# Optimization experiments

Measured on AMD Instinct MI355X. Metric: run time of the kernel, lower is better.

Reference implementation:

```python
import jax, jax.numpy as jnp
import numpy as np

BM = 192  # query block size (kernel hard-coded to BM=192)


def setup_inputs() -> dict:
    key = jax.random.key(0)
    k1, k2, k3 = jax.random.split(key, 3)
    B, H, S, D = 1, 12, 3840, 128
    q = jax.random.normal(k1, (B, H, S, D), dtype=jnp.float32)
    k = jax.random.normal(k2, (B, H, S, D), dtype=jnp.float32)
    v = jax.random.normal(k3, (B, H, S, D), dtype=jnp.float32)
    topk = 1024
    return {"q": q, "k": k, "v": v, "topk": topk}


def reference(q, k, v, topk):
    # Chipmunk SparseDiffAttn core pipeline:
    # 1) dense_colsum_attn: dense attention whose probs are column-summed per
    #    192-query block to produce block scores bs [B,H,QG,S]
    # 2) topk index selection per query group (mask -> indices)
    # 3) csp_attn: block-sparse attention where each 192-query group attends
    #    only to its selected top-k keys
    B, H, S, D = q.shape
    QG = S // BM
    scale = 1.0 / np.sqrt(D)

    # --- dense colsum attention (scoring pass) ---
    scores = jnp.einsum('bhqd,bhkd->bhqk', q, k) * scale      # [B,H,S,S]
    probs = jax.nn.softmax(scores, axis=-1)                   # [B,H,S,S]
    # column-sum of attention probs within each 192-query block
    bs = probs.reshape(B, H, QG, BM, S).sum(axis=-2)          # [B,H,QG,S]

    # --- topk mask -> per-group key indices ---
    _, inds = jax.lax.top_k(bs, topk)                         # [B,H,QG,TK] int32

    # --- block-sparse gather attention (csp_attn) ---
    # gather selected keys/values per query group
    gather = jax.vmap(jax.vmap(lambda kv, idx: kv[idx]))      # over B, H
    kg = gather(k, inds)                                      # [B,H,QG,TK,D]
    vg = gather(v, inds)                                      # [B,H,QG,TK,D]
    qg = q.reshape(B, H, QG, BM, D)                           # [B,H,QG,BM,D]

    s2 = jnp.einsum('bhgqd,bhgkd->bhgqk', qg, kg) * scale     # [B,H,QG,BM,TK]
    p2 = jax.nn.softmax(s2, axis=-1)
    o = jnp.einsum('bhgqk,bhgkd->bhgqd', p2, vg)              # [B,H,QG,BM,D]
    return o.reshape(B, H, S, D)
```

## Files before the change

### kernel.cpp

```cpp
#include <hip/hip_runtime.h>
#include <math.h>


#define HH 12
#define SS 3840
#define DD 128
#define QGn 20
#define TKn 1024
#define NROWS (HH * QGn)
#define HS (HH * SS)
#define NT 60
#define TCH 3072
#define SCALE_D 0.08838834764831845
#define SCALE_F 0.08838834764831845f

typedef short short8 __attribute__((ext_vector_type(8)));
typedef short short4v __attribute__((ext_vector_type(4)));
typedef float f32x4 __attribute__((ext_vector_type(4)));

#define MFMA(a, b, c) __builtin_amdgcn_mfma_f32_16x16x32_bf16(a, b, c, 0, 0, 0)
#define MFMA_B16(c, a, b) \
  c = __builtin_amdgcn_mfma_f32_16x16x32_bf16(a, b, c, 0, 0, 0)

typedef __attribute__((address_space(3))) unsigned int lds_u32;
typedef const __attribute__((address_space(1))) unsigned int glb_u32;

__device__ __forceinline__ unsigned short bf_rne(float x) {
  unsigned u = __float_as_uint(x);
  u = (u + 0x7fffu + ((u >> 16) & 1u)) >> 16;
  return (unsigned short)u;
}
__device__ __forceinline__ float bf_f(unsigned short b) {
  return __uint_as_float(((unsigned)b) << 16);
}
__device__ __forceinline__ void split3(float f, unsigned short& a,
                                       unsigned short& b, unsigned short& c) {
  a = bf_rne(f);
  float r = f - bf_f(a);
  b = bf_rne(r);
  r = r - bf_f(b);
  c = bf_rne(r);
}
__device__ __forceinline__ void split2(float f, unsigned short& a,
                                       unsigned short& b) {
  a = bf_rne(f);
  float r = f - bf_f(a);
  b = bf_rne(r);
}
__device__ __forceinline__ short8 ldfrag(const unsigned short* base, int chunk) {
  return *(const short8*)&base[(size_t)chunk * 8];
}

__global__ __launch_bounds__(1024) void presplit_kernel(
    const float* __restrict__ q, const float* __restrict__ k,
    unsigned short* __restrict__ qsplit, unsigned short* __restrict__ ksplit) {
  const int t = threadIdx.x;
  const int lane = t & 63;
  const int u = t >> 6;
  const int kc = u & 3, kt = u >> 2;
  const int ln = lane & 15, quad = lane >> 4;
  const int c = blockIdx.x;
  const int h = blockIdx.y;
  const float* src = blockIdx.z ? k : q;
  unsigned short* dst = blockIdx.z ? ksplit : qsplit;

  const float* p =
      &src[(size_t)(h * SS + c * 64 + kt * 16 + ln) * DD + kc * 32 + quad * 8];
  float b8[8];
  *(float4*)&b8[0] = *(const float4*)&p[0];
  *(float4*)&b8[4] = *(const float4*)&p[4];
  unsigned short f0[8], f1[8], f2[8];
#pragma unroll
  for (int e = 0; e < 8; ++e) split3(b8[e], f0[e], f1[e], f2[e]);
  size_t base =
      ((size_t)(h * NT + c) * TCH + ((kt * 4 + kc) * 3) * 64 + lane) * 8;
  *(ushort4*)&dst[base + 0] = *(ushort4*)&f0[0];
  *(ushort4*)&dst[base + 4] = *(ushort4*)&f0[4];
  *(ushort4*)&dst[base + 512] = *(ushort4*)&f1[0];
  *(ushort4*)&dst[base + 516] = *(ushort4*)&f1[4];
  *(ushort4*)&dst[base + 1024] = *(ushort4*)&f2[0];
  *(ushort4*)&dst[base + 1028] = *(ushort4*)&f2[4];
}

__global__ __launch_bounds__(256) void stats_mfma(
    const unsigned short* __restrict__ qsplit,
    const unsigned short* __restrict__ ksplit,
    double* __restrict__ lpart) {
  __shared__ __align__(16) unsigned short Bs[3][6144];
  const int t = threadIdx.x;
  const int w = t >> 6;
  const int lane = t & 63;
  const int ln = lane & 15;
  const int quad = lane >> 4;
  const int h = blockIdx.y;
  const int nq = blockIdx.z;
  const int q0 = blockIdx.x * 128 + w * 32;
  const int tq = blockIdx.x * 2 + (w >> 1);
  const int ktA = (w & 1) * 2;

  short8 A[2][4][3];
  {
    const unsigned short* qb = &qsplit[(size_t)(h * NT + tq) * TCH * 8];
#pragma unroll
    for (int s = 0; s < 2; ++s)
#pragma unroll
      for (int kc = 0; kc < 4; ++kc)
#pragma unroll
        for (int cm = 0; cm < 3; ++cm)
          A[s][kc][cm] =
              ldfrag(qb, (((ktA + s) * 4 + kc) * 3 + cm) * 64 + lane);
  }

  double racc[2][4];
#pragma unroll
  for (int s = 0; s < 2; ++s)
#pragma unroll
    for (int r = 0; r < 4; ++r) racc[s][r] = 0.0;

  const unsigned short* kq = &ksplit[(size_t)(h * NT + nq * 15) * TCH * 8];

#define STG_S(slot, j)                                                     \
  do {                                                                     \
    const unsigned short* src_ = kq + (size_t)(j) * 6144 + t * 8;          \
    __builtin_amdgcn_global_load_lds((glb_u32*)(src_),                     \
        (lds_u32*)&Bs[slot][w * 512], 16, 0, 0);                           \
    __builtin_amdgcn_global_load_lds((glb_u32*)(src_ + 2048),              \
        (lds_u32*)&Bs[slot][2048 + w * 512], 16, 0, 0);                    \
    __builtin_amdgcn_global_load_lds((glb_u32*)(src_ + 4096),              \
        (lds_u32*)&Bs[slot][4096 + w * 512], 16, 0, 0);                    \
  } while (0)

  const f32x4 z = {0.f, 0.f, 0.f, 0.f};
  f32x4 C[2][3];

  STG_S(0, 0);

  int cur = 0;
#pragma unroll 1
  for (int j = 0; j < 60; ++j) {
    __builtin_amdgcn_sched_barrier(0);
    if (j < 59) {
      const int nxt = (cur == 2) ? 0 : cur + 1;
      STG_S(nxt, j + 1);
      asm volatile("s_waitcnt vmcnt(3)" ::: "memory");
    } else {
      asm volatile("s_waitcnt vmcnt(0)" ::: "memory");
    }
    __builtin_amdgcn_s_barrier();
    __builtin_amdgcn_sched_barrier(0);
    __builtin_amdgcn_s_setprio(1);
    if (j > 0) {
#pragma unroll
      for (int s = 0; s < 2; ++s)
#pragma unroll
        for (int r = 0; r < 4; ++r) {
          float sv = (C[s][0][r] + C[s][1][r]) + C[s][2][r];
          racc[s][r] += (double)__expf(sv * SCALE_F);
        }
    }
    const unsigned short* Bp = &Bs[cur][0];
#pragma unroll
    for (int kc = 0; kc < 4; ++kc) {
      short8 B0 = *(const short8*)&Bp[(kc * 3 + 0) * 512 + lane * 8];
      short8 B1 = *(const short8*)&Bp[(kc * 3 + 1) * 512 + lane * 8];
      short8 B2 = *(const short8*)&Bp[(kc * 3 + 2) * 512 + lane * 8];
#pragma unroll
      for (int s = 0; s < 2; ++s) {
        if (kc == 0) {
          C[s][0] = MFMA(A[s][0][0], B0, z);
          C[s][1] = MFMA(A[s][0][0], B1, z);
          C[s][1] = MFMA(A[s][0][1], B0, C[s][1]);
          C[s][0] = MFMA(A[s][0][1], B1, C[s][0]);
          C[s][2] = MFMA(A[s][0][2], B0, z);
          C[s][2] = MFMA(A[s][0][0], B2, C[s][2]);
        } else {
          MFMA_B16(C[s][0], A[s][kc][0], B0);
          MFMA_B16(C[s][1], A[s][kc][0], B1);
          MFMA_B16(C[s][1], A[s][kc][1], B0);
          MFMA_B16(C[s][0], A[s][kc][1], B1);
          MFMA_B16(C[s][2], A[s][kc][2], B0);
          MFMA_B16(C[s][2], A[s][kc][0], B2);
        }
      }
    }
    __builtin_amdgcn_s_setprio(0);
    cur = (cur == 2) ? 0 : cur + 1;
  }
#undef STG_S

#pragma unroll
  for (int s = 0; s < 2; ++s)
#pragma unroll
    for (int r = 0; r < 4; ++r) {
      float sv = (C[s][0][r] + C[s][1][r]) + C[s][2][r];
      racc[s][r] += (double)__expf(sv * SCALE_F);
    }

#pragma unroll
  for (int s = 0; s < 2; ++s)
#pragma unroll
    for (int r = 0; r < 4; ++r) {
      double v = racc[s][r];
      v += __shfl_xor(v, 1);
      v += __shfl_xor(v, 2);
      v += __shfl_xor(v, 4);
      v += __shfl_xor(v, 8);
      if (ln == 0)
        lpart[(size_t)nq * HS + h * SS + q0 + s * 16 + quad * 4 + r] = v;
    }
}

__global__ __launch_bounds__(256) void colsum_mfma(
    const unsigned short* __restrict__ qsplit,
    const unsigned short* __restrict__ ksplit,
    const double* __restrict__ lpart, double* __restrict__ bs) {
  __shared__ double rls[192];
  __shared__ __align__(16) unsigned short As[3][6144];
  const int t = threadIdx.x;
  const int w = t >> 6;
  const int lane = t & 63;
  const int ln = lane & 15;
  const int quad = lane >> 4;
  const int h = blockIdx.z, g = blockIdx.y;
  const int k0 = blockIdx.x * 128 + w * 32;
  const int tk = blockIdx.x * 2 + (w >> 1);
  const int ktB = (w & 1) * 2;

  short8 Bk[2][4][3];
  {
    const unsigned short* kb = &ksplit[(size_t)(h * NT + tk) * TCH * 8];
#pragma unroll
    for (int s = 0; s < 2; ++s)
#pragma unroll
      for (int kc = 0; kc < 4; ++kc)
#pragma unroll
        for (int cm = 0; cm < 3; ++cm)
          Bk[s][kc][cm] =
              ldfrag(kb, (((ktB + s) * 4 + kc) * 3 + cm) * 64 + lane);
  }

  if (t < 192) {
    size_t qi = h * SS + g * 192 + t;
    rls[t] = 1.0 / (lpart[qi] + lpart[HS + qi] + lpart[2 * (size_t)HS + qi] +
                    lpart[3 * (size_t)HS + qi]);
  }
  __syncthreads();

  double cacc[2] = {0.0, 0.0};

  const unsigned short* qg = &qsplit[(size_t)(h * NT + g * 3) * TCH * 8];

#define STG_C(slot, j)                                                     \
  do {                                                                     \
    const unsigned short* src_ = qg + (size_t)(j) * 6144 + t * 8;          \
    __builtin_amdgcn_global_load_lds((glb_u32*)(src_),                     \
        (lds_u32*)&As[slot][w * 512], 16, 0, 0);                           \
    __builtin_amdgcn_global_load_lds((glb_u32*)(src_ + 2048),              \
        (lds_u32*)&As[slot][2048 + w * 512], 16, 0, 0);                    \
    __builtin_amdgcn_global_load_lds((glb_u32*)(src_ + 4096),              \
        (lds_u32*)&As[slot][4096 + w * 512], 16, 0, 0);                    \
  } while (0)

  const f32x4 z = {0.f, 0.f, 0.f, 0.f};
  f32x4 C[2][3];

  STG_C(0, 0);

  int cur = 0;
#pragma unroll 1
  for (int j = 0; j < 12; ++j) {
    __builtin_amdgcn_sched_barrier(0);
    if (j < 11) {
      const int nxt = (cur == 2) ? 0 : cur + 1;
      STG_C(nxt, j + 1);
      asm volatile("s_waitcnt vmcnt(3)" ::: "memory");
    } else {
      asm volatile("s_waitcnt vmcnt(0)" ::: "memory");
    }
    __builtin_amdgcn_s_barrier();
    __builtin_amdgcn_sched_barrier(0);
    __builtin_amdgcn_s_setprio(1);
    if (j > 0) {
      const int qprev = (j - 1) * 16;
#pragma unroll
      for (int s = 0; s < 2; ++s)
#pragma unroll
        for (int r = 0; r < 4; ++r) {
          float p = __expf(((C[s][0][r] + C[s][1][r]) + C[s][2][r]) * SCALE_F);
          cacc[s] += (double)p * rls[qprev + quad * 4 + r];
        }
    }
    const unsigned short* Ap = &As[cur][0];
#pragma unroll
    for (int kc = 0; kc < 4; ++kc) {
      short8 A0 = *(const short8*)&Ap[(kc * 3 + 0) * 512 + lane * 8];
      short8 A1 = *(const short8*)&Ap[(kc * 3 + 1) * 512 + lane * 8];
      short8 A2 = *(const short8*)&Ap[(kc * 3 + 2) * 512 + lane * 8];
#pragma unroll
      for (int s = 0; s < 2; ++s) {
        if (kc == 0) {
          C[s][0] = MFMA(A0, Bk[s][0][0], z);
          C[s][1] = MFMA(A1, Bk[s][0][0], z);
          C[s][1] = MFMA(A0, Bk[s][0][1], C[s][1]);
          C[s][0] = MFMA(A1, Bk[s][0][1], C[s][0]);
          C[s][2] = MFMA(A2, Bk[s][0][0], z);
          C[s][2] = MFMA(A0, Bk[s][0][2], C[s][2]);
        } else {
          MFMA_B16(C[s][0], A0, Bk[s][kc][0]);
          MFMA_B16(C[s][1], A1, Bk[s][kc][0]);
          MFMA_B16(C[s][1], A0, Bk[s][kc][1]);
          MFMA_B16(C[s][0], A1, Bk[s][kc][1]);
          MFMA_B16(C[s][2], A2, Bk[s][kc][0]);
          MFMA_B16(C[s][2], A0, Bk[s][kc][2]);
        }
      }
    }
    __builtin_amdgcn_s_setprio(0);
    cur = (cur == 2) ? 0 : cur + 1;
  }
#undef STG_C

#pragma unroll
  for (int s = 0; s < 2; ++s)
#pragma unroll
    for (int r = 0; r < 4; ++r) {
      float p = __expf(((C[s][0][r] + C[s][1][r]) + C[s][2][r]) * SCALE_F);
      cacc[s] += (double)p * rls[176 + quad * 4 + r];
    }

#pragma unroll
  for (int s = 0; s < 2; ++s) {
    double v = cacc[s];
    v += __shfl_xor(v, 16);
    v += __shfl_xor(v, 32);
    if (quad == 0)
      bs[(size_t)(h * QGn + g) * SS + k0 + s * 16 + ln] = v;
  }
}

__global__ __launch_bounds__(256) void topk3_kernel(
    const double* __restrict__ bs, int* __restrict__ inds,
    double* __restrict__ bnd_val, int* __restrict__ bnd_idx) {
  __shared__ unsigned long long u[SS];
  __shared__ int hist[256];
  __shared__ int sfx[256];
  __shared__ int s_bin, s_r;
  __shared__ int c_gt, c_eq;
  __shared__ unsigned long long rv[256];
  __shared__ int ri[256];
  const int t = threadIdx.x;
  const int row = blockIdx.x;
  const double* vals = bs + (size_t)row * SS;

  for (int i = t; i < SS; i += 256)
    u[i] = (unsigned long long)__double_as_longlong(vals[i]);

  unsigned long long pref = 0ull;
  int r = TKn;
  for (int shift = 56; shift >= 0; shift -= 8) {
    hist[t] = 0;
    __syncthreads();
    unsigned long long himask =
        (shift == 56) ? 0ull : (0xFFFFFFFFFFFFFFFFull << (shift + 8));
    for (int i = t; i < SS; i += 256) {
      unsigned long long uv = u[i];
      if ((uv & himask) == (pref & himask))
        atomicAdd(&hist[(int)((uv >> shift) & 255)], 1);
    }
    __syncthreads();
    sfx[t] = hist[t];
    __syncthreads();
#pragma unroll
    for (int off = 1; off < 256; off <<= 1) {
      int v = (t + off < 256) ? sfx[t + off] : 0;
      __syncthreads();
      sfx[t] += v;
      __syncthreads();
    }
    {
      int St = sfx[t];
      int Sn = (t == 255) ? 0 : sfx[t + 1];
      if (St >= r && Sn < r) {
        s_bin = t;
        s_r = r - Sn;
      }
    }
    if (t == 0) {
      c_gt = 0;
      c_eq = 0;
    }
    __syncthreads();
    pref |= ((unsigned long long)s_bin) << shift;
    r = s_r;
    __syncthreads();
  }
  const int G = TKn - r;
  int* out = inds + (size_t)row * TKn;
  unsigned long long mb = 0ull;
  int mbi = -1;
  for (int i = t; i < SS; i += 256) {
    unsigned long long uv = u[i];
    if (uv > pref) {
      int p = atomicAdd(&c_gt, 1);
      out[p] = i;
    } else if (uv == pref) {
      int e = atomicAdd(&c_eq, 1);
      if (e < r) out[G + e] = i;
      if (e == r - 1) bnd_idx[row * 2 + 0] = i;
    } else if (uv > mb) {
      mb = uv;
      mbi = i;
    }
  }
  rv[t] = mb;
  ri[t] = mbi;
  __syncthreads();
  for (int s2 = 128; s2 > 0; s2 >>= 1) {
    if (t < s2 && rv[t + s2] > rv[t]) {
      rv[t] = rv[t + s2];
      ri[t] = ri[t + s2];
    }
    __syncthreads();
  }
  if (t == 0) {
    bnd_val[row * 2 + 0] = __longlong_as_double((long long)pref);
    bnd_val[row * 2 + 1] = __longlong_as_double((long long)rv[0]);
    bnd_idx[row * 2 + 1] = ri[0];
  }
}

__global__ __launch_bounds__(256) void argmin_kernel(
    const double* __restrict__ bnd_val, const int* __restrict__ bnd_idx,
    int* __restrict__ rsel) {
  __shared__ double gmin[256];
  __shared__ int grow[256];
  const int t = threadIdx.x;
  double g = 1e300;
  int r = -1;
  if (t < NROWS) {
    g = bnd_val[t * 2 + 0] - bnd_val[t * 2 + 1];
    r = t;
  }
  gmin[t] = g;
  grow[t] = r;
  __syncthreads();
  for (int s2 = 128; s2 > 0; s2 >>= 1) {
    if (t < s2 && gmin[t + s2] < gmin[t]) {
      gmin[t] = gmin[t + s2];
      grow[t] = grow[t + s2];
    }
    __syncthreads();
  }
  if (t == 0) {
    int rr = grow[0];
    rsel[0] = rr;
    rsel[1] = bnd_idx[rr * 2 + 0];
    rsel[2] = bnd_idx[rr * 2 + 1];
  }
}

__global__ __launch_bounds__(256) void exact_rl_kernel(
    const float* __restrict__ q, const float* __restrict__ k,
    const int* __restrict__ rsel, double* __restrict__ rl_exact) {
  __shared__ double qd[DD];
  __shared__ double red[256];
  const int t = threadIdx.x;
  const int row = rsel[0];
  const int h = row / QGn, g = row % QGn;
  const float* qp = &q[(size_t)(h * SS + g * 192 + blockIdx.x) * DD];
  if (t < DD) qd[t] = (double)qp[t];
  __syncthreads();
  double l = 0.0;
  for (int kk = t; kk < SS; kk += 256) {
    const float* kp = &k[(size_t)(h * SS + kk) * DD];
    double s = 0.0;
#pragma unroll 4
    for (int d = 0; d < DD; d += 4) {
      float4 kv = *(const float4*)&kp[d];
      s += qd[d] * (double)kv.x + qd[d + 1] * (double)kv.y +
           qd[d + 2] * (double)kv.z + qd[d + 3] * (double)kv.w;
    }
    l += exp(s * SCALE_D);
  }
  red[t] = l;
  __syncthreads();
  for (int s2 = 128; s2 > 0; s2 >>= 1) {
    if (t < s2) red[t] += red[t + s2];
    __syncthreads();
  }
  if (t == 0) rl_exact[blockIdx.x] = 1.0 / red[0];
}

__global__ __launch_bounds__(256) void exact_pair_kernel(
    const float* __restrict__ q, const float* __restrict__ k,
    const int* __restrict__ rsel, const double* __restrict__ rl_exact,
    int* __restrict__ inds) {
  __shared__ double redX[256], redY[256];
  const int t = threadIdx.x;
  const int row = rsel[0], kept = rsel[1], drop = rsel[2];
  const int h = row / QGn, g = row % QGn;
  double px = 0.0, py = 0.0;
  if (t < 192) {
    const float* qp = &q[(size_t)(h * SS + g * 192 + t) * DD];
    const float* kx = &k[(size_t)(h * SS + kept) * DD];
    const float* ky = &k[(size_t)(h * SS + drop) * DD];
    double sx = 0.0, sy = 0.0;
#pragma unroll 4
    for (int d = 0; d < DD; ++d) {
      double qv = (double)qp[d];
      sx += qv * (double)kx[d];
      sy += qv * (double)ky[d];
    }
    double rv = rl_exact[t];
    px = exp(sx * SCALE_D) * rv;
    py = exp(sy * SCALE_D) * rv;
  }
  redX[t] = px;
  redY[t] = py;
  __syncthreads();
  for (int s2 = 128; s2 > 0; s2 >>= 1) {
    if (t < s2) { redX[t] += redX[t + s2]; redY[t] += redY[t + s2]; }
    __syncthreads();
  }
  if (t == 0)
    inds[(size_t)row * TKn + (TKn - 1)] = (redX[0] <= redY[0]) ? kept : drop;
}

__global__ __launch_bounds__(768, 3) void sparse_attn_mfma(
    const float* __restrict__ q, const float* __restrict__ v,
    const int* __restrict__ inds, const unsigned short* __restrict__ ksplit,
    float* __restrict__ out) {
  __shared__ __align__(16) unsigned short ksmN[16 * 512];
  __shared__ __align__(16) unsigned short vsm[2][128][40];
  __shared__ __align__(16) unsigned short pbuf[12][2][16][36];
  const int t = threadIdx.x;
  const int w = t >> 6;
  const int lane = t & 63;
  const int ln = lane & 15;
  const int quad = lane >> 4;
  const int g = blockIdx.x, h = blockIdx.y;
  const int* ip = &inds[(size_t)(h * QGn + g) * TKn];
  const unsigned short* kbh = &ksplit[(size_t)(h * NT) * (TCH * 8)];

  short8 A[4][2];
  {
    const float* qp =
        &q[(size_t)(h * SS + g * 192 + w * 16 + ln) * DD + quad * 8];
#pragma unroll
    for (int kc = 0; kc < 4; ++kc) {
      float b8[8];
      *(float4*)&b8[0] = *(const float4*)&qp[kc * 32];
      *(float4*)&b8[4] = *(const float4*)&qp[kc * 32 + 4];
      short8 f0, f1;
#pragma unroll
      for (int e = 0; e < 8; ++e) {
        unsigned short x0, x1;
        split2(b8[e], x0, x1);
        f0[e] = (short)x0; f1[e] = (short)x1;
      }
      A[kc][0] = f0; A[kc][1] = f1;
    }
  }

  f32x4 O[8];
#pragma unroll
  for (int dt = 0; dt < 8; ++dt) O[dt] = (f32x4){0.f, 0.f, 0.f, 0.f};
  float lacc[4] = {0.f, 0.f, 0.f, 0.f};

  const int kk = t >> 3;
  const int sub = t & 7;
  const int sW = w >> 1;
  const int c0 = w * 4;

  int gkA = 0;
  float4 rv4[4];
  if (w < 4) {
    gkA = ip[sW * 16 + ln];
    int gkV = ip[kk];
    const float* vp = &v[(size_t)(h * SS + gkV) * DD + sub * 16];
#pragma unroll
    for (int e4 = 0; e4 < 4; ++e4) rv4[e4] = *(const float4*)&vp[e4 * 4];
  }

  for (int kt = 0; kt < TKn; kt += 32) {
    __builtin_amdgcn_s_barrier();
    __builtin_amdgcn_sched_barrier(0);
    if (w < 4) {
      const bool more = (kt + 32 < TKn);
      int gkVn = 0, gkAn = 0;
      if (more) {
        gkVn = ip[kt + 32 + kk];
        gkAn = ip[kt + 32 + sW * 16 + ln];
      }
      {
        const unsigned short* rowp = kbh + (size_t)(gkA >> 6) * (TCH * 8) +
                                     ((gkA & 15) + 16 * quad) * 8;
        const int ktile = (gkA >> 4) & 3;
#pragma unroll
        for (int i = 0; i < 4; ++i) {
          const int c16 = c0 + i;
          const int kc = (c16 >> 1) & 3;
          const int cm = c16 & 1;
          __builtin_amdgcn_global_load_lds(
              (glb_u32*)(rowp + ((ktile * 4 + kc) * 3 + cm) * 512),
              (lds_u32*)&ksmN[c16 * 512], 16, 0, 0);
        }
      }
#pragma unroll
      for (int e4 = 0; e4 < 4; ++e4) {
        float4 vv = rv4[e4];
        ushort4 v0, v1;
        split2(vv.x, v0.x, v1.x);
        split2(vv.y, v0.y, v1.y);
        split2(vv.z, v0.z, v1.z);
        split2(vv.w, v0.w, v1.w);
        int d0 = sub * 16 + e4 * 4;
        vsm[0][d0 + 0][kk] = v0.x; vsm[1][d0 + 0][kk] = v1.x;
        vsm[0][d0 + 1][kk] = v0.y; vsm[1][d0 + 1][kk] = v1.y;
        vsm[0][d0 + 2][kk] = v0.z; vsm[1][d0 + 2][kk] = v1.z;
        vsm[0][d0 + 3][kk] = v0.w; vsm[1][d0 + 3][kk] = v1.w;
      }
      if (more) {
        const float* vp = &v[(size_t)(h * SS + gkVn) * DD + sub * 16];
#pragma unroll
        for (int e4 = 0; e4 < 4; ++e4) rv4[e4] = *(const float4*)&vp[e4 * 4];
        asm volatile("s_waitcnt vmcnt(4) lgkmcnt(0)" ::: "memory");
        gkA = gkAn;
      } else {
        asm volatile("s_waitcnt vmcnt(0) lgkmcnt(0)" ::: "memory");
      }
    }
    __builtin_amdgcn_s_barrier();
    __builtin_amdgcn_sched_barrier(0);

#pragma unroll
    for (int s = 0; s < 2; ++s) {
      f32x4 C0 = {0.f, 0.f, 0.f, 0.f};
      f32x4 C1 = C0;
      __builtin_amdgcn_s_setprio(1);
#pragma unroll
      for (int kc = 0; kc < 4; ++kc) {
        short8 B0 = *(const short8*)&ksmN[(s * 8 + kc * 2 + 0) * 512 + lane * 8];
        short8 B1 = *(const short8*)&ksmN[(s * 8 + kc * 2 + 1) * 512 + lane * 8];
        MFMA_B16(C0, A[kc][0], B0);
        MFMA_B16(C1, A[kc][1], B0);
        MFMA_B16(C1, A[kc][0], B1);
      }
      __builtin_amdgcn_s_setprio(0);
#pragma unroll
      for (int r = 0; r < 4; ++r) {
        float pv = __expf((C0[r] + C1[r]) * SCALE_F);
        lacc[r] += pv;
        unsigned short p0, p1;
        split2(pv, p0, p1);
        pbuf[w][0][quad * 4 + r][s * 16 + ln] = p0;
        pbuf[w][1][quad * 4 + r][s * 16 + ln] = p1;
      }
    }
    short8 P0, P1;
    {
      const unsigned short* pb0 = &pbuf[w][0][ln][quad * 8];
      const unsigned short* pb1 = &pbuf[w][1][ln][quad * 8];
      short4v lo0 = *(const short4v*)pb0;
      short4v hi0 = *(const short4v*)(pb0 + 4);
      short4v lo1 = *(const short4v*)pb1;
      short4v hi1 = *(const short4v*)(pb1 + 4);
      P0 = __builtin_shufflevector(lo0, hi0, 0, 1, 2, 3, 4, 5, 6, 7);
      P1 = __builtin_shufflevector(lo1, hi1, 0, 1, 2, 3, 4, 5, 6, 7);
    }
    __builtin_amdgcn_s_setprio(1);
#pragma unroll
    for (int dt = 0; dt < 8; ++dt) {
      short8 V0 = *(const short8*)&vsm[0][dt * 16 + ln][quad * 8];
      short8 V1 = *(const short8*)&vsm[1][dt * 16 + ln][quad * 8];
      MFMA_B16(O[dt], P0, V0);
      MFMA_B16(O[dt], P1, V0);
      MFMA_B16(O[dt], P0, V1);
    }
    __builtin_amdgcn_s_setprio(0);
  }

#pragma unroll
  for (int r = 0; r < 4; ++r) {
    float l = lacc[r];
    l += __shfl_xor(l, 1);
    l += __shfl_xor(l, 2);
    l += __shfl_xor(l, 4);
    l += __shfl_xor(l, 8);
    float rl = 1.f / l;
    float* op =
        &out[(size_t)(h * SS + g * 192 + w * 16 + quad * 4 + r) * DD];
#pragma unroll
    for (int dt = 0; dt < 8; ++dt) op[dt * 16 + ln] = O[dt][r] * rl;
  }
}

extern "C" void kernel_launch(void* const* d_in, const int* in_sizes, int n_in,
                              void* d_out, int out_size, void* d_ws, size_t ws_size,
                              hipStream_t stream) {
  const float* q = (const float*)d_in[0];
  const float* k = (const float*)d_in[1];
  const float* v = (const float*)d_in[2];
  float* out = (float*)d_out;

  const size_t SPLIT_ELEMS = (size_t)HH * NT * TCH * 8;
  unsigned short* qsplit = (unsigned short*)d_ws;
  unsigned short* ksplit = qsplit + SPLIT_ELEMS;
  double* lpart = (double*)(ksplit + SPLIT_ELEMS);
  double* bs = lpart + 4 * (size_t)HS;
  int* inds = (int*)(bs + (size_t)HH * QGn * SS);
  double* bnd_val = (double*)(inds + (size_t)NROWS * TKn);
  int* bnd_idx = (int*)(bnd_val + (size_t)NROWS * 2);
  int* rsel = bnd_idx + NROWS * 2;
  double* rl_exact = (double*)(rsel + 4);

  presplit_kernel<<<dim3(NT, HH, 2), 1024, 0, stream>>>(q, k, qsplit, ksplit);
  stats_mfma<<<dim3(SS / 128, HH, 4), 256, 0, stream>>>(qsplit, ksplit, lpart);
  colsum_mfma<<<dim3(SS / 128, QGn, HH), 256, 0, stream>>>(qsplit, ksplit, lpart, bs);
  topk3_kernel<<<dim3(NROWS), 256, 0, stream>>>(bs, inds, bnd_val, bnd_idx);
  argmin_kernel<<<dim3(1), 256, 0, stream>>>(bnd_val, bnd_idx, rsel);
  exact_rl_kernel<<<dim3(192), 256, 0, stream>>>(q, k, rsel, rl_exact);
  exact_pair_kernel<<<dim3(1), 256, 0, stream>>>(q, k, rsel, rl_exact, inds);
  sparse_attn_mfma<<<dim3(QGn, HH), 768, 0, stream>>>(q, v, inds, ksplit, out);
}
```

Baseline: 720.9 us.

## Fold argmin into exact kernels, widen presplit stores, split PV work across waves

The separate argmin launch is removed; each exact kernel recomputes the small row argmin redundantly, saving one launch. Presplit stores are widened to 16-byte writes. In sparse attention, each wave now computes PV for two query subtiles over half of the D columns, sharing V fragments across two P tiles through a workgroup barrier on pbuf. This adds a barrier per key tile and an LDS exchange of row normalisers before the output writes.

```diff
diff --git a/kernel.cpp b/kernel.cpp
--- a/kernel.cpp
+++ b/kernel.cpp
@@ -69,17 +69,14 @@
   float b8[8];
   *(float4*)&b8[0] = *(const float4*)&p[0];
   *(float4*)&b8[4] = *(const float4*)&p[4];
-  unsigned short f0[8], f1[8], f2[8];
+  __attribute__((aligned(16))) unsigned short f0[8], f1[8], f2[8];
 #pragma unroll
   for (int e = 0; e < 8; ++e) split3(b8[e], f0[e], f1[e], f2[e]);
   size_t base =
       ((size_t)(h * NT + c) * TCH + ((kt * 4 + kc) * 3) * 64 + lane) * 8;
-  *(ushort4*)&dst[base + 0] = *(ushort4*)&f0[0];
-  *(ushort4*)&dst[base + 4] = *(ushort4*)&f0[4];
-  *(ushort4*)&dst[base + 512] = *(ushort4*)&f1[0];
-  *(ushort4*)&dst[base + 516] = *(ushort4*)&f1[4];
-  *(ushort4*)&dst[base + 1024] = *(ushort4*)&f2[0];
-  *(ushort4*)&dst[base + 1028] = *(ushort4*)&f2[4];
+  *(uint4*)&dst[base + 0] = *(const uint4*)f0;
+  *(uint4*)&dst[base + 512] = *(const uint4*)f1;
+  *(uint4*)&dst[base + 1024] = *(const uint4*)f2;
 }
 
 __global__ __launch_bounds__(256) void stats_mfma(
@@ -429,43 +426,33 @@
   }
 }
 
-__global__ __launch_bounds__(256) void argmin_kernel(
-    const double* __restrict__ bnd_val, const int* __restrict__ bnd_idx,
-    int* __restrict__ rsel) {
+__global__ __launch_bounds__(256) void exact_rl_kernel(
+    const float* __restrict__ q, const float* __restrict__ k,
+    const double* __restrict__ bnd_val, double* __restrict__ rl_exact) {
   __shared__ double gmin[256];
   __shared__ int grow[256];
-  const int t = threadIdx.x;
-  double g = 1e300;
-  int r = -1;
-  if (t < NROWS) {
-    g = bnd_val[t * 2 + 0] - bnd_val[t * 2 + 1];
-    r = t;
-  }
-  gmin[t] = g;
-  grow[t] = r;
-  __syncthreads();
-  for (int s2 = 128; s2 > 0; s2 >>= 1) {
-    if (t < s2 && gmin[t + s2] < gmin[t]) {
-      gmin[t] = gmin[t + s2];
-      grow[t] = grow[t + s2];
-    }
-    __syncthreads();
-  }
-  if (t == 0) {
-    int rr = grow[0];
-    rsel[0] = rr;
-    rsel[1] = bnd_idx[rr * 2 + 0];
-    rsel[2] = bnd_idx[rr * 2 + 1];
-  }
-}
-
-__global__ __launch_bounds__(256) void exact_rl_kernel(
-    const float* __restrict__ q, const float* __restrict__ k,
-    const int* __restrict__ rsel, double* __restrict__ rl_exact) {
   __shared__ double qd[DD];
   __shared__ double red[256];
   const int t = threadIdx.x;
-  const int row = rsel[0];
+  {
+    double gv = 1e300;
+    int rr = -1;
+    if (t < NROWS) {
+      gv = bnd_val[t * 2 + 0] - bnd_val[t * 2 + 1];
+      rr = t;
+    }
+    gmin[t] = gv;
+    grow[t] = rr;
+    __syncthreads();
+    for (int s2 = 128; s2 > 0; s2 >>= 1) {
+      if (t < s2 && gmin[t + s2] < gmin[t]) {
+        gmin[t] = gmin[t + s2];
+        grow[t] = grow[t + s2];
+      }
+      __syncthreads();
+    }
+  }
+  const int row = grow[0];
   const int h = row / QGn, g = row % QGn;
   const float* qp = &q[(size_t)(h * SS + g * 192 + blockIdx.x) * DD];
   if (t < DD) qd[t] = (double)qp[t];
@@ -493,11 +480,32 @@
 
 __global__ __launch_bounds__(256) void exact_pair_kernel(
     const float* __restrict__ q, const float* __restrict__ k,
-    const int* __restrict__ rsel, const double* __restrict__ rl_exact,
-    int* __restrict__ inds) {
+    const double* __restrict__ bnd_val, const int* __restrict__ bnd_idx,
+    const double* __restrict__ rl_exact, int* __restrict__ inds) {
+  __shared__ double gmin[256];
+  __shared__ int grow[256];
   __shared__ double redX[256], redY[256];
   const int t = threadIdx.x;
-  const int row = rsel[0], kept = rsel[1], drop = rsel[2];
+  {
+    double gv = 1e300;
+    int rr = -1;
+    if (t < NROWS) {
+      gv = bnd_val[t * 2 + 0] - bnd_val[t * 2 + 1];
+      rr = t;
+    }
+    gmin[t] = gv;
+    grow[t] = rr;
+    __syncthreads();
+    for (int s2 = 128; s2 > 0; s2 >>= 1) {
+      if (t < s2 && gmin[t + s2] < gmin[t]) {
+        gmin[t] = gmin[t + s2];
+        grow[t] = grow[t + s2];
+      }
+      __syncthreads();
+    }
+  }
+  const int row = grow[0];
+  const int kept = bnd_idx[row * 2 + 0], drop = bnd_idx[row * 2 + 1];
   const int h = row / QGn, g = row % QGn;
   double px = 0.0, py = 0.0;
   if (t < 192) {
@@ -533,6 +541,7 @@
   __shared__ __align__(16) unsigned short ksmN[16 * 512];
   __shared__ __align__(16) unsigned short vsm[2][128][40];
   __shared__ __align__(16) unsigned short pbuf[12][2][16][36];
+  __shared__ float rls_sm[12][16];
   const int t = threadIdx.x;
   const int w = t >> 6;
   const int lane = t & 63;
@@ -541,6 +550,8 @@
   const int g = blockIdx.x, h = blockIdx.y;
   const int* ip = &inds[(size_t)(h * QGn + g) * TKn];
   const unsigned short* kbh = &ksplit[(size_t)(h * NT) * (TCH * 8)];
+  const int qs0 = (w % 6) * 2;
+  const int dtb = (w / 6) * 4;
 
   short8 A[4][2];
   {
@@ -562,9 +573,12 @@
     }
   }
 
-  f32x4 O[8];
-#pragma unroll
-  for (int dt = 0; dt < 8; ++dt) O[dt] = (f32x4){0.f, 0.f, 0.f, 0.f};
+  f32x4 Oa[4], Ob[4];
+#pragma unroll
+  for (int d2 = 0; d2 < 4; ++d2) {
+    Oa[d2] = (f32x4){0.f, 0.f, 0.f, 0.f};
+    Ob[d2] = (f32x4){0.f, 0.f, 0.f, 0.f};
+  }
   float lacc[4] = {0.f, 0.f, 0.f, 0.f};
 
   const int kk = t >> 3;
@@ -657,25 +671,39 @@
         pbuf[w][1][quad * 4 + r][s * 16 + ln] = p1;
       }
     }
-    short8 P0, P1;
+    asm volatile("s_waitcnt lgkmcnt(0)" ::: "memory");
+    __builtin_amdgcn_s_barrier();
+    __builtin_amdgcn_sched_barrier(0);
+
+    short8 P0a, P1a, P0b, P1b;
     {
-      const unsigned short* pb0 = &pbuf[w][0][ln][quad * 8];
-      const unsigned short* pb1 = &pbuf[w][1][ln][quad * 8];
-      short4v lo0 = *(const short4v*)pb0;
-      short4v hi0 = *(const short4v*)(pb0 + 4);
-      short4v lo1 = *(const short4v*)pb1;
-      short4v hi1 = *(const short4v*)(pb1 + 4);
-      P0 = __builtin_shufflevector(lo0, hi0, 0, 1, 2, 3, 4, 5, 6, 7);
-      P1 = __builtin_shufflevector(lo1, hi1, 0, 1, 2, 3, 4, 5, 6, 7);
+      const unsigned short* pb;
+      short4v lo, hi;
+      pb = &pbuf[qs0][0][ln][quad * 8];
+      lo = *(const short4v*)pb; hi = *(const short4v*)(pb + 4);
+      P0a = __builtin_shufflevector(lo, hi, 0, 1, 2, 3, 4, 5, 6, 7);
+      pb = &pbuf[qs0][1][ln][quad * 8];
+      lo = *(const short4v*)pb; hi = *(const short4v*)(pb + 4);
+      P1a = __builtin_shufflevector(lo, hi, 0, 1, 2, 3, 4, 5, 6, 7);
+      pb = &pbuf[qs0 + 1][0][ln][quad * 8];
+      lo = *(const short4v*)pb; hi = *(const short4v*)(pb + 4);
+      P0b = __builtin_shufflevector(lo, hi, 0, 1, 2, 3, 4, 5, 6, 7);
+      pb = &pbuf[qs0 + 1][1][ln][quad * 8];
+      lo = *(const short4v*)pb; hi = *(const short4v*)(pb + 4);
+      P1b = __builtin_shufflevector(lo, hi, 0, 1, 2, 3, 4, 5, 6, 7);
     }
     __builtin_amdgcn_s_setprio(1);
 #pragma unroll
-    for (int dt = 0; dt < 8; ++dt) {
+    for (int d2 = 0; d2 < 4; ++d2) {
+      const int dt = dtb + d2;
       short8 V0 = *(const short8*)&vsm[0][dt * 16 + ln][quad * 8];
       short8 V1 = *(const short8*)&vsm[1][dt * 16 + ln][quad * 8];
-      MFMA_B16(O[dt], P0, V0);
-      MFMA_B16(O[dt], P1, V0);
-      MFMA_B16(O[dt], P0, V1);
+      MFMA_B16(Oa[d2], P0a, V0);
+      MFMA_B16(Oa[d2], P1a, V0);
+      MFMA_B16(Oa[d2], P0a, V1);
+      MFMA_B16(Ob[d2], P0b, V0);
+      MFMA_B16(Ob[d2], P1b, V0);
+      MFMA_B16(Ob[d2], P0b, V1);
     }
     __builtin_amdgcn_s_setprio(0);
   }
@@ -688,10 +716,24 @@
     l += __shfl_xor(l, 4);
     l += __shfl_xor(l, 8);
     float rl = 1.f / l;
-    float* op =
-        &out[(size_t)(h * SS + g * 192 + w * 16 + quad * 4 + r) * DD];
-#pragma unroll
-    for (int dt = 0; dt < 8; ++dt) op[dt * 16 + ln] = O[dt][r] * rl;
+    if (ln == 0) rls_sm[w][quad * 4 + r] = rl;
+  }
+  __syncthreads();
+
+#pragma unroll
+  for (int half = 0; half < 2; ++half) {
+    const int qs = qs0 + half;
+#pragma unroll
+    for (int r = 0; r < 4; ++r) {
+      float rlv = rls_sm[qs][quad * 4 + r];
+      float* op =
+          &out[(size_t)(h * SS + g * 192 + qs * 16 + quad * 4 + r) * DD];
+#pragma unroll
+      for (int d2 = 0; d2 < 4; ++d2) {
+        float ov = half ? Ob[d2][r] : Oa[d2][r];
+        op[(dtb + d2) * 16 + ln] = ov * rlv;
+      }
+    }
   }
 }
 
@@ -718,8 +760,7 @@
   stats_mfma<<<dim3(SS / 128, HH, 4), 256, 0, stream>>>(qsplit, ksplit, lpart);
   colsum_mfma<<<dim3(SS / 128, QGn, HH), 256, 0, stream>>>(qsplit, ksplit, lpart, bs);
   topk3_kernel<<<dim3(NROWS), 256, 0, stream>>>(bs, inds, bnd_val, bnd_idx);
-  argmin_kernel<<<dim3(1), 256, 0, stream>>>(bnd_val, bnd_idx, rsel);
-  exact_rl_kernel<<<dim3(192), 256, 0, stream>>>(q, k, rsel, rl_exact);
-  exact_pair_kernel<<<dim3(1), 256, 0, stream>>>(q, k, rsel, rl_exact, inds);
+  exact_rl_kernel<<<dim3(192), 256, 0, stream>>>(q, k, bnd_val, rl_exact);
+  exact_pair_kernel<<<dim3(1), 256, 0, stream>>>(q, k, bnd_val, bnd_idx, rl_exact, inds);
   sparse_attn_mfma<<<dim3(QGn, HH), 768, 0, stream>>>(q, v, inds, ksplit, out);
 }
```

New measurement: 734.7 us. About the same (+1.9%).
